# Optimization experiments

Measured on AMD Instinct MI355X. Metric: run time of the kernel, lower is better.

## Reference

```python
import jax, jax.numpy as jnp
import numpy as np

N = 4096        # batch_size per view
D = 256         # embed_dim
TEMPERATURE = 0.1


def setup_inputs() -> dict:
    key = jax.random.key(0)
    k1, k2 = jax.random.split(key)
    return {
        "z_i": jax.random.normal(k1, (N, D), dtype=jnp.float32),
        "z_j": jax.random.normal(k2, (N, D), dtype=jnp.float32),
    }


def reference(z_i, z_j):
    n = z_i.shape[0]
    # L2-normalize each row (CosineSimilarity == dot of normalized vectors)
    zi = z_i * jax.lax.rsqrt(jnp.sum(z_i * z_i, axis=1, keepdims=True))
    zj = z_j * jax.lax.rsqrt(jnp.sum(z_j * z_j, axis=1, keepdims=True))
    r = jnp.concatenate([zj, zi], axis=0)               # [2n, d], order matches torch cat([z_j, z_i])
    S = (r @ r.T) / TEMPERATURE                          # [2n, 2n] normalized GEMM, no O(n^2 d) broadcast

    idx = jnp.arange(2 * n)
    pos_col = (idx + n) % (2 * n)                        # positive partner: diag(+n) / diag(-n)
    pos = S[idx, pos_col]                                # [2n]

    # Faithful mask: the original masks the diagonal AND both full cross blocks,
    # so negatives are same-view off-diagonal entries only. Keep = negatives + positive.
    same_block = (idx[:, None] // n) == (idx[None, :] // n)
    keep = (same_block & (idx[:, None] != idx[None, :])) | (idx[None, :] == pos_col[:, None])

    # CrossEntropy with label 0 and reduction='sum', then / (2n)  ==  mean(logsumexp - pos)
    lse = jax.nn.logsumexp(jnp.where(keep, S, -jnp.inf), axis=1)  # [2n]
    return jnp.mean(lse - pos)
```

## Files before the change

kernel.cpp:

```cpp
#include <hip/hip_runtime.h>
#include <math.h>

#define N_ROWS 4096
#define DIM 256
constexpr float INV_T = 10.0f;

#define NT 32
#define NTILES 528
#define BM 128
#define BK 64
#define PSTRIDE 512

typedef __attribute__((ext_vector_type(8))) short short8;
typedef __attribute__((ext_vector_type(4))) float floatx4;

__device__ __forceinline__ unsigned short f2bf(float f) {
    unsigned int u = __float_as_uint(f);
    return (unsigned short)((u + 0x7FFFu + ((u >> 16) & 1u)) >> 16);
}

__global__ __launch_bounds__(256) void normalize_kernel(
    const float* __restrict__ z_i, const float* __restrict__ z_j,
    unsigned short* __restrict__ R0, unsigned short* __restrict__ R1,
    float* __restrict__ pos, float* __restrict__ out)
{
    if (blockIdx.x == 0 && threadIdx.x == 0) out[0] = 0.0f;

    int wave = threadIdx.x >> 6;
    int lane = threadIdx.x & 63;
    int row = blockIdx.x * 4 + wave;

    float4 a = ((const float4*)(z_i + (size_t)row * DIM))[lane];
    float4 b = ((const float4*)(z_j + (size_t)row * DIM))[lane];

    float ssa = a.x*a.x + a.y*a.y + a.z*a.z + a.w*a.w;
    float ssb = b.x*b.x + b.y*b.y + b.z*b.z + b.w*b.w;
    float dab = a.x*b.x + a.y*b.y + a.z*b.z + a.w*b.w;
    #pragma unroll
    for (int off = 1; off < 64; off <<= 1) {
        ssa += __shfl_xor(ssa, off);
        ssb += __shfl_xor(ssb, off);
        dab += __shfl_xor(dab, off);
    }
    float ra = rsqrtf(ssa);
    float rb = rsqrtf(ssb);

    ushort4 ua, ub;
    ua.x = f2bf(a.x * ra); ua.y = f2bf(a.y * ra); ua.z = f2bf(a.z * ra); ua.w = f2bf(a.w * ra);
    ub.x = f2bf(b.x * rb); ub.y = f2bf(b.y * rb); ub.z = f2bf(b.z * rb); ub.w = f2bf(b.w * rb);
    ((ushort4*)(R1 + (size_t)row * DIM))[lane] = ua;
    ((ushort4*)(R0 + (size_t)row * DIM))[lane] = ub;

    if (lane == 0) pos[row] = dab * ra * rb * INV_T;
}

__global__ __launch_bounds__(256) void gemm_sym(
    const unsigned short* __restrict__ R0,
    const unsigned short* __restrict__ R1,
    float* __restrict__ part)
{
    __shared__ unsigned short As[BM * BK];
    __shared__ unsigned short Bs[BM * BK];

    int view = blockIdx.y;
    const unsigned short* R = view ? R1 : R0;
    float* P = part + (size_t)(view * NTILES + blockIdx.x) * PSTRIDE;

    int t = blockIdx.x;
    int by = 0;
    while (t >= NT - by) { t -= NT - by; ++by; }
    int bx = by + t;
    int rT = by * BM, cT = bx * BM;

    int tid = threadIdx.x;
    int lane = tid & 63;
    int wave = tid >> 6;
    int wy = wave >> 1, wx = wave & 1;
    int m = lane & 15, q = lane >> 4;

    floatx4 acc[4][4] = {};

    for (int kidx = 0; kidx < 4; ++kidx) {
        int k0 = kidx * BK;
        __syncthreads();
        #pragma unroll
        for (int it = 0; it < 4; ++it) {
            int s = it * 256 + tid;
            int row = s >> 3, c = s & 7;
            uint4 va = *(const uint4*)(R + (size_t)(rT + row) * DIM + k0 + c * 8);
            uint4 vb = *(const uint4*)(R + (size_t)(cT + row) * DIM + k0 + c * 8);
            int slot = row * 8 + (c ^ (row & 7));
            *(uint4*)&As[slot * 8] = va;
            *(uint4*)&Bs[slot * 8] = vb;
        }
        __syncthreads();

        #pragma unroll
        for (int kk = 0; kk < 2; ++kk) {
            short8 af[4], bfr[4];
            #pragma unroll
            for (int tt = 0; tt < 4; ++tt) {
                int ra = wy * 64 + tt * 16 + m;
                af[tt] = *(const short8*)&As[(ra * 8 + ((kk * 4 + q) ^ (ra & 7))) * 8];
                int rb = wx * 64 + tt * 16 + m;
                bfr[tt] = *(const short8*)&Bs[(rb * 8 + ((kk * 4 + q) ^ (rb & 7))) * 8];
            }
            #pragma unroll
            for (int i = 0; i < 4; ++i)
                #pragma unroll
                for (int j = 0; j < 4; ++j)
                    acc[i][j] = __builtin_amdgcn_mfma_f32_16x16x32_bf16(af[i], bfr[j], acc[i][j], 0, 0, 0);
        }
    }

    float rs[4][4] = {};
    float cs[4] = {0.f, 0.f, 0.f, 0.f};
    #pragma unroll
    for (int i = 0; i < 4; ++i) {
        #pragma unroll
        for (int j = 0; j < 4; ++j) {
            int gcol = cT + wx * 64 + j * 16 + m;
            #pragma unroll
            for (int r = 0; r < 4; ++r) {
                int grow = rT + wy * 64 + i * 16 + q * 4 + r;
                float e = (grow == gcol) ? 0.0f : __expf(acc[i][j][r] * INV_T);
                rs[i][r] += e;
                cs[j] += e;
            }
        }
    }
    #pragma unroll
    for (int off = 1; off < 16; off <<= 1)
        #pragma unroll
        for (int i = 0; i < 4; ++i)
            #pragma unroll
            for (int r = 0; r < 4; ++r)
                rs[i][r] += __shfl_xor(rs[i][r], off);
    if (m == 0) {
        #pragma unroll
        for (int i = 0; i < 4; ++i) {
            float4 v = make_float4(rs[i][0], rs[i][1], rs[i][2], rs[i][3]);
            *(float4*)&P[wx * 128 + wy * 64 + i * 16 + q * 4] = v;
        }
    }
    #pragma unroll
    for (int off = 16; off < 64; off <<= 1)
        #pragma unroll
        for (int j = 0; j < 4; ++j)
            cs[j] += __shfl_xor(cs[j], off);
    if (q == 0) {
        #pragma unroll
        for (int j = 0; j < 4; ++j)
            P[256 + wy * 128 + wx * 64 + j * 16 + m] = (bx == by) ? 0.0f : cs[j];
    }
}

__global__ __launch_bounds__(256) void finalize_kernel(
    const float* __restrict__ part, const float* __restrict__ pos,
    float* __restrict__ out)
{
    int g = blockIdx.x * 256 + threadIdx.x;
    int v = g >> 12, r = g & (N_ROWS - 1);
    int b = r >> 7, l = r & 127;
    const float* P = part + (size_t)v * NTILES * PSTRIDE;

    float d = 0.f;
    int t0 = b * NT - (b * (b - 1)) / 2;
    for (int k = 0; k < NT - b; ++k) {
        const float* T = P + (size_t)(t0 + k) * PSTRIDE;
        d += T[l] + T[128 + l];
    }
    for (int by = 0; by <= b; ++by) {
        int tb = by * NT - (by * (by - 1)) / 2 + (b - by);
        const float* T = P + (size_t)tb * PSTRIDE;
        d += T[256 + l] + T[384 + l];
    }
    float p = pos[r];
    float s = __logf(d + __expf(p)) - p;
    #pragma unroll
    for (int off = 1; off < 64; off <<= 1) s += __shfl_xor(s, off);
    if ((threadIdx.x & 63) == 0)
        atomicAdd(out, s * (1.0f / (2 * N_ROWS)));
}

extern "C" void kernel_launch(void* const* d_in, const int* in_sizes, int n_in,
                              void* d_out, int out_size, void* d_ws, size_t ws_size,
                              hipStream_t stream) {
    const float* z_i = (const float*)d_in[0];
    const float* z_j = (const float*)d_in[1];
    char* ws = (char*)d_ws;
    unsigned short* R0 = (unsigned short*)ws;
    unsigned short* R1 = (unsigned short*)(ws + (2u << 20));
    float* pos  = (float*)(ws + (4u << 20));
    float* part = (float*)(ws + (4u << 20) + (64u << 10));

    normalize_kernel<<<N_ROWS / 4, 256, 0, stream>>>(z_i, z_j, R0, R1, pos,
                                                     (float*)d_out);
    dim3 grid(NTILES, 2);
    gemm_sym<<<grid, 256, 0, stream>>>(R0, R1, part);
    finalize_kernel<<<2 * N_ROWS / 256, 256, 0, stream>>>(part, pos, (float*)d_out);
}
```

Baseline: 91.36 us.

## Load MFMA fragments directly from global memory with register double buffering

Removes the LDS staging and both block barriers from the symmetric GEMM. Each wave now loads its bf16 A/B fragments straight from global memory into registers, prefetching the next 32-wide k slice while MFMAs run on the current one. This drops shared-memory traffic and synchronisation. In exchange, the two waves that share a tile row or column load the same data twice, the global loads are less coalesced (16-byte pieces spread across rows), and the doubled fragment registers may lower occupancy.

```diff
diff --git a/kernel.cpp b/kernel.cpp
--- a/kernel.cpp
+++ b/kernel.cpp
@@ -8,7 +8,6 @@
 #define NT 32
 #define NTILES 528
 #define BM 128
-#define BK 64
 #define PSTRIDE 512
 
 typedef __attribute__((ext_vector_type(8))) short short8;
@@ -59,9 +58,6 @@
     const unsigned short* __restrict__ R1,
     float* __restrict__ part)
 {
-    __shared__ unsigned short As[BM * BK];
-    __shared__ unsigned short Bs[BM * BK];
-
     int view = blockIdx.y;
     const unsigned short* R = view ? R1 : R0;
     float* P = part + (size_t)(view * NTILES + blockIdx.x) * PSTRIDE;
@@ -78,39 +74,34 @@
     int wy = wave >> 1, wx = wave & 1;
     int m = lane & 15, q = lane >> 4;
 
+    const unsigned short* Abase = R + (size_t)(rT + wy * 64 + m) * DIM + q * 8;
+    const unsigned short* Bbase = R + (size_t)(cT + wx * 64 + m) * DIM + q * 8;
+
     floatx4 acc[4][4] = {};
+    short8 fa[2][4], fb[2][4];
 
-    for (int kidx = 0; kidx < 4; ++kidx) {
-        int k0 = kidx * BK;
-        __syncthreads();
-        #pragma unroll
-        for (int it = 0; it < 4; ++it) {
-            int s = it * 256 + tid;
-            int row = s >> 3, c = s & 7;
-            uint4 va = *(const uint4*)(R + (size_t)(rT + row) * DIM + k0 + c * 8);
-            uint4 vb = *(const uint4*)(R + (size_t)(cT + row) * DIM + k0 + c * 8);
-            int slot = row * 8 + (c ^ (row & 7));
-            *(uint4*)&As[slot * 8] = va;
-            *(uint4*)&Bs[slot * 8] = vb;
-        }
-        __syncthreads();
+    #pragma unroll
+    for (int tt = 0; tt < 4; ++tt) {
+        fa[0][tt] = *(const short8*)(Abase + (size_t)tt * 16 * DIM);
+        fb[0][tt] = *(const short8*)(Bbase + (size_t)tt * 16 * DIM);
+    }
 
-        #pragma unroll
-        for (int kk = 0; kk < 2; ++kk) {
-            short8 af[4], bfr[4];
+    #pragma unroll
+    for (int kk = 0; kk < 8; ++kk) {
+        int cur = kk & 1, nxt = cur ^ 1;
+        if (kk < 7) {
+            int ko = (kk + 1) * 32;
             #pragma unroll
             for (int tt = 0; tt < 4; ++tt) {
-                int ra = wy * 64 + tt * 16 + m;
-                af[tt] = *(const short8*)&As[(ra * 8 + ((kk * 4 + q) ^ (ra & 7))) * 8];
-                int rb = wx * 64 + tt * 16 + m;
-                bfr[tt] = *(const short8*)&Bs[(rb * 8 + ((kk * 4 + q) ^ (rb & 7))) * 8];
+                fa[nxt][tt] = *(const short8*)(Abase + (size_t)tt * 16 * DIM + ko);
+                fb[nxt][tt] = *(const short8*)(Bbase + (size_t)tt * 16 * DIM + ko);
             }
+        }
+        #pragma unroll
+        for (int i = 0; i < 4; ++i)
             #pragma unroll
-            for (int i = 0; i < 4; ++i)
-                #pragma unroll
-                for (int j = 0; j < 4; ++j)
-                    acc[i][j] = __builtin_amdgcn_mfma_f32_16x16x32_bf16(af[i], bfr[j], acc[i][j], 0, 0, 0);
-        }
+            for (int j = 0; j < 4; ++j)
+                acc[i][j] = __builtin_amdgcn_mfma_f32_16x16x32_bf16(fa[cur][i], fb[cur][j], acc[i][j], 0, 0, 0);
     }
 
     float rs[4][4] = {};
```

Measured after the change: 110.6 us. 1.21x slower.
